# Performance work log

Hardware: AMD Instinct MI355X
Metric: run time of the kernel (lower is better)

Reference implementation:

```python
import jax, jax.numpy as jnp
import numpy as np

SPACE = 63
STRIDE = 2
TEMP = 0.07
W_CHAR, W_WORD, W_PHRASE, W_IDEA = 1.0, 0.5, 0.1, 0.1


def setup_inputs() -> dict:
    key = jax.random.key(0)
    ks = jax.random.split(key, 6)
    B, S, V, D = 8, 4096, 256, 512
    return {
        "logits": jax.random.normal(ks[0], (B, S, V), jnp.float32),
        "word_preds": jax.random.normal(ks[1], (B, D, S // STRIDE), jnp.float32),
        "char_features": jax.random.normal(ks[2], (B, D, S), jnp.float32),
        "contrastive_2": jax.random.normal(ks[3], (B, 128, 1024), jnp.float32),
        "contrastive_3": jax.random.normal(ks[4], (B, 128, 256), jnp.float32),
        "targets": jax.random.randint(ks[5], (B, S), 0, V, jnp.int32),
        "mask": jnp.ones((B, S), jnp.float32),
    }


def _info_nce(emb, temp=TEMP):
    # emb: (B, dim, L). Anchors = even positions, positives = odd positions.
    B, dim, L = emb.shape
    n_pairs = L // 2
    a = emb[:, :, 0:2 * n_pairs:2].transpose(0, 2, 1).reshape(-1, dim)
    p = emb[:, :, 1:2 * n_pairs:2].transpose(0, 2, 1).reshape(-1, dim)
    a = a / jnp.maximum(jnp.linalg.norm(a, axis=1, keepdims=True), 1e-12)
    p = p / jnp.maximum(jnp.linalg.norm(p, axis=1, keepdims=True), 1e-12)
    logits = (a @ p.T) / temp  # (n, n)
    n = logits.shape[0]
    logp = jax.nn.log_softmax(logits, axis=1)
    idx = jnp.arange(n)
    return -jnp.mean(logp[idx, idx])


def _word_span_loss(word_preds, char_features, targets, stride=STRIDE):
    # Segment-mean over spans between consecutive spaces; MSE vs gathered preds.
    B, D, S = char_features.shape
    Wlen = word_preds.shape[2]
    nseg = S + 2  # segment k in [1, n_spaces-1] = span after the k-th space; last slot = junk
    space = targets == SPACE
    cs = jnp.cumsum(space.astype(jnp.int32), axis=1)  # inclusive space count
    seg = jnp.where(space, nseg - 1, cs)          # non-space chars -> span id
    seg_sp = jnp.where(space, cs, nseg - 1)       # space positions -> their space index k
    t_idx = jnp.arange(S, dtype=jnp.int32)

    def per_batch(feats, seg_b, seg_sp_b):
        sums = jax.ops.segment_sum(feats.T, seg_b, num_segments=nseg)  # (nseg, D)
        cnts = jax.ops.segment_sum(jnp.ones((S,), feats.dtype), seg_b, num_segments=nseg)
        pos = jnp.full((nseg,), S, jnp.int32).at[seg_sp_b].set(t_idx)  # position of k-th space
        return sums, cnts, pos

    sums, cnts, pos = jax.vmap(per_batch)(char_features, seg, seg_sp)
    n_sp = cs[:, -1]  # (B,)
    k = jnp.arange(nseg)[None, :]
    valid = (k >= 1) & (k <= n_sp[:, None] - 1) & (cnts > 0) & ((pos // stride) < Wlen)
    means = jax.lax.stop_gradient(sums / jnp.maximum(cnts, 1.0)[..., None])  # target.detach()
    wp = jnp.clip(pos // stride, 0, Wlen - 1)  # (B, nseg)
    preds = jnp.take_along_axis(word_preds.transpose(0, 2, 1), wp[:, :, None], axis=1)  # (B,nseg,D)
    mse = jnp.mean((preds - means) ** 2, axis=-1)  # per-span F.mse_loss (mean over feat dim)
    tot = jnp.sum(jnp.where(valid, mse, 0.0))
    cnt = jnp.sum(valid).astype(mse.dtype)
    return jnp.where(cnt > 0, tot / jnp.maximum(cnt, 1.0), 0.0)


def reference(logits, word_preds, char_features, contrastive_2, contrastive_3, targets, mask):
    # char CE with mask
    logp = jax.nn.log_softmax(logits, axis=-1)
    ce = -jnp.take_along_axis(logp, targets[..., None].astype(jnp.int32), axis=-1)[..., 0]
    n = jnp.sum(mask)
    char_loss = jnp.where(n > 0, jnp.sum(ce * mask) / jnp.maximum(n, 1.0), jnp.mean(ce))
    word_loss = _word_span_loss(word_preds, char_features, targets)
    phrase_loss = _info_nce(contrastive_2)
    idea_loss = _info_nce(contrastive_3)
    return (W_CHAR * char_loss + W_WORD * word_loss
            + W_PHRASE * phrase_loss + W_IDEA * idea_loss)
```

## Files before the change

### kernel.cpp

```cpp
#include <hip/hip_runtime.h>

#define SPACE_TOK 63
#define INV_T 14.285714285714286f
#define SA_SCALE 20.609929155556595f
#define LN2F 0.6931471805599453f

typedef __attribute__((ext_vector_type(8))) short bf16x8;
typedef __attribute__((ext_vector_type(4))) float f32x4;

#define O_CECM   0
#define O_CEM    4096
#define O_CEC    8192
#define O_WPART  12288
#define O_WCNT   14336
#define O_PEXP2  14464
#define O_DIAG2  145536
#define O_PEXP3  161920
#define O_DIAG3  194688
#define O_A2     198784
#define SZ_A2    (4096*128*2)
#define O_P2     (O_A2 + SZ_A2)
#define O_A3     (O_P2 + SZ_A2)
#define SZ_A3    (1024*128*2)
#define O_P3     (O_A3 + SZ_A3)

#define SMEM_A 18048

__device__ inline unsigned short f2bf(float x) {
  union { float f; unsigned int u; } c; c.f = x;
  unsigned int r = c.u + 0x7fffu + ((c.u >> 16) & 1u);
  return (unsigned short)(r >> 16);
}

__device__ void norm_body(char* smem, const float* __restrict__ emb, int L,
                          unsigned short* __restrict__ Abf, unsigned short* __restrict__ Pbf,
                          int b, int l0) {
  float (*tile)[33] = (float(*)[33])smem;
  float (*np8)[32]  = (float(*)[32])(smem + 16896);
  float* scl        = (float*)(smem + 16896 + 1024);
  int tid = threadIdx.x;
  int lx = tid & 31, cq = tid >> 5;
  const float* eb = emb + (size_t)b * 128 * L + l0;
  for (int c = cq; c < 128; c += 8) tile[c][lx] = eb[(size_t)c * L + lx];
  __syncthreads();
  {
    float s = 0.f;
    for (int c = cq; c < 128; c += 8) { float x = tile[c][lx]; s += x * x; }
    np8[cq][lx] = s;
  }
  __syncthreads();
  if (tid < 32) {
    float t = 0.f;
#pragma unroll
    for (int g = 0; g < 8; ++g) t += np8[g][tid];
    float nrm = fmaxf(sqrtf(t), 1e-12f);
    scl[tid] = ((tid & 1) ? 1.0f : SA_SCALE) / nrm;
  }
  __syncthreads();
  int c = tid & 127, lh = tid >> 7;
  int half = L >> 1;
  for (int lp = lh; lp < 32; lp += 2) {
    int l = l0 + lp;
    int row = b * half + (l >> 1);
    unsigned short v = f2bf(tile[c][lp] * scl[lp]);
    ((l & 1) ? Pbf : Abf)[(size_t)row * 128 + c] = v;
  }
}

__device__ void ce_body(char* smem, const float* __restrict__ logits,
                        const int* __restrict__ targets, const float* __restrict__ mask,
                        char* ws, int cb) {
  int tid = threadIdx.x;
  int wave = tid >> 6, lane = tid & 63;
  int rbase = cb * 32 + wave * 8;
  float4 v[8];
  float mk[8];
  int tg[8];
#pragma unroll
  for (int rr = 0; rr < 8; ++rr) v[rr] = ((const float4*)logits)[(size_t)(rbase + rr) * 64 + lane];
#pragma unroll
  for (int rr = 0; rr < 8; ++rr) { tg[rr] = targets[rbase + rr]; mk[rr] = mask[rbase + rr]; }
  float aCM = 0.f, aM = 0.f, aC = 0.f;
#pragma unroll
  for (int rr = 0; rr < 8; ++rr) {
    float e = __expf(v[rr].x) + __expf(v[rr].y) + __expf(v[rr].z) + __expf(v[rr].w);
#pragma unroll
    for (int m = 1; m < 64; m <<= 1) e += __shfl_xor(e, m);
    int t = tg[rr];
    int q = t & 3;
    float sel = (q == 0) ? v[rr].x : (q == 1) ? v[rr].y : (q == 2) ? v[rr].z : v[rr].w;
    float xt = __shfl(sel, t >> 2);
    float ce = __logf(e) - xt;
    aCM += ce * mk[rr]; aM += mk[rr]; aC += ce;
  }
  float (*red)[3] = (float(*)[3])smem;
  if (lane == 0) { red[wave][0] = aCM; red[wave][1] = aM; red[wave][2] = aC; }
  __syncthreads();
  if (tid == 0) {
    ((float*)(ws + O_CECM))[cb] = red[0][0] + red[1][0] + red[2][0] + red[3][0];
    ((float*)(ws + O_CEM ))[cb] = red[0][1] + red[1][1] + red[2][1] + red[3][1];
    ((float*)(ws + O_CEC ))[cb] = red[0][2] + red[1][2] + red[2][2] + red[3][2];
  }
}

__global__ void __launch_bounds__(256) fusedA_kernel(const float* __restrict__ logits,
                                                     const int* __restrict__ targets,
                                                     const float* __restrict__ mask,
                                                     const float* __restrict__ c2,
                                                     const float* __restrict__ c3,
                                                     char* __restrict__ ws) {
  extern __shared__ char smem[];
  int bid = blockIdx.x;
  if (bid < 256) {
    norm_body(smem, c2, 1024, (unsigned short*)(ws + O_A2), (unsigned short*)(ws + O_P2),
              bid & 7, (bid >> 3) * 32);
  } else if (bid < 320) {
    int nb = bid - 256;
    norm_body(smem, c3, 256, (unsigned short*)(ws + O_A3), (unsigned short*)(ws + O_P3),
              nb & 7, (nb >> 3) * 32);
  } else {
    ce_body(smem, logits, targets, mask, ws, bid - 320);
  }
}

__global__ void __launch_bounds__(256) word_kernel(const float* __restrict__ wp,
                                                   const float* __restrict__ cf,
                                                   const int* __restrict__ targets,
                                                   char* __restrict__ ws) {
  __shared__ int sc[256];
  __shared__ int splist[1024];
  __shared__ int snext_sh;
  __shared__ float wacc[4];
  int tid = threadIdx.x;
  int w = blockIdx.x;
  int z = w & 15, tq = (w >> 4) & 3, b = w >> 6;
  const int* tb = targets + b * 4096;
  int tbase = tq * 1024;
  int4 tok = ((const int4*)(tb + tbase))[tid];
  int f0 = (tok.x == SPACE_TOK), f1 = (tok.y == SPACE_TOK),
      f2 = (tok.z == SPACE_TOK), f3 = (tok.w == SPACE_TOK);
  int cnt = f0 + f1 + f2 + f3;
  sc[tid] = cnt;
  __syncthreads();
  for (int off = 1; off < 256; off <<= 1) {
    int v = (tid >= off) ? sc[tid - off] : 0;
    __syncthreads();
    sc[tid] += v;
    __syncthreads();
  }
  int base = sc[tid] - cnt;
  int p = tbase + tid * 4;
  if (f0) splist[base++] = p;
  if (f1) splist[base++] = p + 1;
  if (f2) splist[base++] = p + 2;
  if (f3) splist[base++] = p + 3;
  int m = sc[255];
  if (tid == 0) snext_sh = -1;
  __syncthreads();
  if (m > 0) {
    for (int wstart = tbase + 1024; wstart < 4096 && snext_sh < 0; wstart += 1024) {
      int t = wstart + tid * 4;
      int4 tk = ((const int4*)tb)[t >> 2];
      int found = 0x7fffffff;
      if (tk.x == SPACE_TOK) found = t;
      else if (tk.y == SPACE_TOK) found = t + 1;
      else if (tk.z == SPACE_TOK) found = t + 2;
      else if (tk.w == SPACE_TOK) found = t + 3;
#pragma unroll
      for (int mm = 1; mm < 64; mm <<= 1) found = min(found, __shfl_xor(found, mm));
      if ((tid & 63) == 0) sc[tid >> 6] = found;
      __syncthreads();
      if (tid == 0) {
        int f = min(min(sc[0], sc[1]), min(sc[2], sc[3]));
        if (f != 0x7fffffff) snext_sh = f;
      }
      __syncthreads();
    }
  }
  int snext = snext_sh;
  int wave = tid >> 6, lane = tid & 63;
  int dbase = z * 32 + wave * 8;
  const float* r0 = cf + ((size_t)(b * 512 + dbase)) * 4096;
  float myacc = 0.f;
  float lcnt = 0.f;
  for (int i = 0; i < m; ++i) {
    int t0 = splist[i];
    int t1 = (i + 1 < m) ? splist[i + 1] : snext;
    if (t1 < 0) break;
    int seglen = t1 - t0 - 1;
    if (seglen <= 0) continue;
    lcnt += 1.0f;
    int wpos = t0 >> 1;
    float invc = 1.0f / (float)seglen;
    int c0 = (t0 + 1) >> 2;
    int c1 = (t1 + 3) >> 2;
    float s0 = 0.f, s1 = 0.f, s2 = 0.f, s3 = 0.f, s4 = 0.f, s5 = 0.f, s6 = 0.f, s7 = 0.f;
    for (int c = c0 + lane; c < c1; c += 64) {
      int tbp = c << 2;
      float4 v0 = *(const float4*)(r0 + 0 * 4096 + tbp);
      float4 v1 = *(const float4*)(r0 + 1 * 4096 + tbp);
      float4 v2 = *(const float4*)(r0 + 2 * 4096 + tbp);
      float4 v3 = *(const float4*)(r0 + 3 * 4096 + tbp);
      float4 v4 = *(const float4*)(r0 + 4 * 4096 + tbp);
      float4 v5 = *(const float4*)(r0 + 5 * 4096 + tbp);
      float4 v6 = *(const float4*)(r0 + 6 * 4096 + tbp);
      float4 v7 = *(const float4*)(r0 + 7 * 4096 + tbp);
      float m0 = (tbp + 0 > t0 && tbp + 0 < t1) ? 1.f : 0.f;
      float m1 = (tbp + 1 > t0 && tbp + 1 < t1) ? 1.f : 0.f;
      float m2 = (tbp + 2 > t0 && tbp + 2 < t1) ? 1.f : 0.f;
      float m3 = (tbp + 3 > t0 && tbp + 3 < t1) ? 1.f : 0.f;
      s0 += v0.x * m0 + v0.y * m1 + v0.z * m2 + v0.w * m3;
      s1 += v1.x * m0 + v1.y * m1 + v1.z * m2 + v1.w * m3;
      s2 += v2.x * m0 + v2.y * m1 + v2.z * m2 + v2.w * m3;
      s3 += v3.x * m0 + v3.y * m1 + v3.z * m2 + v3.w * m3;
      s4 += v4.x * m0 + v4.y * m1 + v4.z * m2 + v4.w * m3;
      s5 += v5.x * m0 + v5.y * m1 + v5.z * m2 + v5.w * m3;
      s6 += v6.x * m0 + v6.y * m1 + v6.z * m2 + v6.w * m3;
      s7 += v7.x * m0 + v7.y * m1 + v7.z * m2 + v7.w * m3;
    }
#pragma unroll
    for (int mm = 1; mm < 64; mm <<= 1) {
      s0 += __shfl_xor(s0, mm); s1 += __shfl_xor(s1, mm);
      s2 += __shfl_xor(s2, mm); s3 += __shfl_xor(s3, mm);
      s4 += __shfl_xor(s4, mm); s5 += __shfl_xor(s5, mm);
      s6 += __shfl_xor(s6, mm); s7 += __shfl_xor(s7, mm);
    }
    if (lane < 8) {
      float sv = (lane == 0) ? s0 : (lane == 1) ? s1 : (lane == 2) ? s2 : (lane == 3) ? s3
               : (lane == 4) ? s4 : (lane == 5) ? s5 : (lane == 6) ? s6 : s7;
      float mean = sv * invc;
      float pred = wp[((size_t)(b * 512 + dbase + lane)) * 2048 + wpos];
      float diff = pred - mean;
      myacc += diff * diff;
    }
  }
#pragma unroll
  for (int mm = 1; mm < 8; mm <<= 1) myacc += __shfl_xor(myacc, mm);
  if (lane == 0) wacc[wave] = myacc;
  __syncthreads();
  if (tid == 0) {
    ((float*)(ws + O_WPART))[w] = (wacc[0] + wacc[1] + wacc[2] + wacc[3]) * (1.0f / 512.0f);
    if (z == 0) ((float*)(ws + O_WCNT))[w >> 4] = lcnt;
  }
}

__device__ void nce_body(char* smem, const unsigned short* __restrict__ A,
                         const unsigned short* __restrict__ P, int n, int sliceJ,
                         int blk_i, int s, float* __restrict__ pexp,
                         float* __restrict__ diag) {
  int tid = threadIdx.x;
  int wave = tid >> 6, lane = tid & 63;
  int col = lane & 15, quad = lane >> 4;
  int I0 = blk_i * 16;
  const unsigned short* Ap = A + (size_t)(I0 + col) * 128 + quad * 8;
  bf16x8 a0 = *(const bf16x8*)(Ap);
  bf16x8 a1 = *(const bf16x8*)(Ap + 32);
  bf16x8 a2 = *(const bf16x8*)(Ap + 64);
  bf16x8 a3 = *(const bf16x8*)(Ap + 96);
  float rl0 = 0.f, rl1 = 0.f, rl2 = 0.f, rl3 = 0.f;
  float dcap = 0.f;
  int perW = sliceJ >> 2;
  int J0w = s * sliceJ + wave * perW, Jend = J0w + perW;
#pragma unroll 2
  for (int J = J0w; J < Jend; J += 16) {
    const unsigned short* Pp = P + (size_t)(J + col) * 128 + quad * 8;
    bf16x8 b0 = *(const bf16x8*)(Pp);
    bf16x8 b1 = *(const bf16x8*)(Pp + 32);
    bf16x8 b2 = *(const bf16x8*)(Pp + 64);
    bf16x8 b3 = *(const bf16x8*)(Pp + 96);
    f32x4 cfr = {0.f, 0.f, 0.f, 0.f};
    cfr = __builtin_amdgcn_mfma_f32_16x16x32_bf16(a0, b0, cfr, 0, 0, 0);
    cfr = __builtin_amdgcn_mfma_f32_16x16x32_bf16(a1, b1, cfr, 0, 0, 0);
    cfr = __builtin_amdgcn_mfma_f32_16x16x32_bf16(a2, b2, cfr, 0, 0, 0);
    cfr = __builtin_amdgcn_mfma_f32_16x16x32_bf16(a3, b3, cfr, 0, 0, 0);
    rl0 += exp2f(cfr[0] - SA_SCALE);
    rl1 += exp2f(cfr[1] - SA_SCALE);
    rl2 += exp2f(cfr[2] - SA_SCALE);
    rl3 += exp2f(cfr[3] - SA_SCALE);
    if (J == I0) {
      int r = col - (quad << 2);
      if (r == 0) dcap = cfr[0];
      else if (r == 1) dcap = cfr[1];
      else if (r == 2) dcap = cfr[2];
      else if (r == 3) dcap = cfr[3];
    }
  }
  float (*part)[16][16] = (float(*)[16][16])smem;
  float (*dpart)[16]    = (float(*)[16])(smem + 4096);
  part[wave][(quad << 2) + 0][col] = rl0;
  part[wave][(quad << 2) + 1][col] = rl1;
  part[wave][(quad << 2) + 2][col] = rl2;
  part[wave][(quad << 2) + 3][col] = rl3;
  if (quad == (col >> 2)) dpart[wave][col] = dcap;
  __syncthreads();
  {
    int rrow = tid >> 4, cc = tid & 15;
    float sv = 0.f, d = 0.f;
#pragma unroll
    for (int ww = 0; ww < 4; ++ww) { sv += part[ww][rrow][cc]; d += dpart[ww][rrow]; }
#pragma unroll
    for (int mm = 1; mm < 16; mm <<= 1) sv += __shfl_xor(sv, mm);
    if (cc == 0) {
      pexp[I0 + rrow] = sv;
      if (I0 >= s * sliceJ && I0 < (s + 1) * sliceJ) diag[I0 + rrow] = d;
    }
  }
}

__global__ void __launch_bounds__(256) fusedC_kernel(char* __restrict__ ws) {
  extern __shared__ char smem[];
  int bid = blockIdx.x;
  if (bid < 2048) {
    nce_body(smem, (const unsigned short*)(ws + O_A2), (const unsigned short*)(ws + O_P2),
             4096, 512, bid >> 3, bid & 7,
             (float*)(ws + O_PEXP2) + (bid & 7) * 4096, (float*)(ws + O_DIAG2));
  } else {
    int nb = bid - 2048;
    nce_body(smem, (const unsigned short*)(ws + O_A3), (const unsigned short*)(ws + O_P3),
             1024, 128, nb >> 3, nb & 7,
             (float*)(ws + O_PEXP3) + (nb & 7) * 1024, (float*)(ws + O_DIAG3));
  }
}

__global__ void __launch_bounds__(256) final_kernel(const char* __restrict__ ws,
                                                    float* __restrict__ out) {
  int tid = threadIdx.x;
  int wave = tid >> 6, lane = tid & 63;
  float v[7] = {0.f, 0.f, 0.f, 0.f, 0.f, 0.f, 0.f};
  {
    float4 a = ((const float4*)(ws + O_CECM))[tid];
    float4 bb = ((const float4*)(ws + O_CEM))[tid];
    float4 c = ((const float4*)(ws + O_CEC))[tid];
    v[0] = a.x + a.y + a.z + a.w;
    v[1] = bb.x + bb.y + bb.z + bb.w;
    v[2] = c.x + c.y + c.z + c.w;
  }
  if (tid < 128) {
    float4 wv = ((const float4*)(ws + O_WPART))[tid];
    v[3] = wv.x + wv.y + wv.z + wv.w;
  }
  if (tid < 32) v[4] = ((const float*)(ws + O_WCNT))[tid];
  for (int r4 = tid; r4 < 1024; r4 += 256) {
    float4 S = {0.f, 0.f, 0.f, 0.f};
#pragma unroll
    for (int s = 0; s < 8; ++s) {
      float4 pv = ((const float4*)(ws + O_PEXP2))[s * 1024 + r4];
      S.x += pv.x; S.y += pv.y; S.z += pv.z; S.w += pv.w;
    }
    float4 dg = ((const float4*)(ws + O_DIAG2))[r4];
    v[5] += 4.0f * INV_T + __logf(S.x) + __logf(S.y) + __logf(S.z) + __logf(S.w)
            - LN2F * (dg.x + dg.y + dg.z + dg.w);
  }
  if (tid < 256) {
    int r4 = tid;
    float4 S = {0.f, 0.f, 0.f, 0.f};
#pragma unroll
    for (int s = 0; s < 8; ++s) {
      float4 pv = ((const float4*)(ws + O_PEXP3))[s * 256 + r4];
      S.x += pv.x; S.y += pv.y; S.z += pv.z; S.w += pv.w;
    }
    float4 dg = ((const float4*)(ws + O_DIAG3))[r4];
    v[6] = 4.0f * INV_T + __logf(S.x) + __logf(S.y) + __logf(S.z) + __logf(S.w)
           - LN2F * (dg.x + dg.y + dg.z + dg.w);
  }
#pragma unroll
  for (int j = 0; j < 7; ++j) {
    float x = v[j];
#pragma unroll
    for (int mm = 1; mm < 64; mm <<= 1) x += __shfl_xor(x, mm);
    v[j] = x;
  }
  __shared__ float fr[4][7];
  if (lane == 0)
#pragma unroll
    for (int j = 0; j < 7; ++j) fr[wave][j] = v[j];
  __syncthreads();
  if (tid == 0) {
    float s[7];
#pragma unroll
    for (int j = 0; j < 7; ++j) s[j] = fr[0][j] + fr[1][j] + fr[2][j] + fr[3][j];
    float n = s[1];
    float charL = (n > 0.f) ? (s[0] / fmaxf(n, 1.f)) : (s[2] / 32768.0f);
    float wordL = (s[4] > 0.f) ? (s[3] / fmaxf(s[4], 1.f)) : 0.f;
    out[0] = charL + 0.5f * wordL + 0.1f * (s[5] / 4096.0f) + 0.1f * (s[6] / 1024.0f);
  }
}

extern "C" void kernel_launch(void* const* d_in, const int* in_sizes, int n_in,
                              void* d_out, int out_size, void* d_ws, size_t ws_size,
                              hipStream_t stream) {
  (void)in_sizes; (void)n_in; (void)out_size; (void)ws_size;
  const float* logits        = (const float*)d_in[0];
  const float* word_preds    = (const float*)d_in[1];
  const float* char_features = (const float*)d_in[2];
  const float* c2            = (const float*)d_in[3];
  const float* c3            = (const float*)d_in[4];
  const int*   targets       = (const int*)d_in[5];
  const float* mask          = (const float*)d_in[6];
  float* out = (float*)d_out;
  char* ws = (char*)d_ws;

  fusedA_kernel<<<1344, 256, SMEM_A, stream>>>(logits, targets, mask, c2, c3, ws);
  word_kernel<<<512, 256, 0, stream>>>(word_preds, char_features, targets, ws);
  fusedC_kernel<<<2560, 256, 4480, stream>>>(ws);
  final_kernel<<<1, 256, 0, stream>>>(ws, out);
}
```

Before: 212.5 us.

## Fuse word, NCE and CE work into one kernel and tile bf16 layout for MFMA

Moves the cross-entropy blocks out of the normalisation kernel and merges the word-span loss, both InfoNCE similarity passes and the CE reduction into a single heterogeneous launch. This cuts one kernel launch and lets memory-bound word/CE blocks overlap with MFMA-bound NCE blocks. The normalised bf16 anchor/positive matrices are now written in a 16-row tiled layout, so each lane's MFMA operand loads are contiguous. The LDS partial-sum array is also padded to avoid bank conflicts. The risk is that the fused kernel needs more shared memory per block, which may lower occupancy for the light blocks.

```diff
diff --git a/kernel.cpp b/kernel.cpp
--- a/kernel.cpp
+++ b/kernel.cpp
@@ -17,7 +17,7 @@
 #define O_DIAG2  145536
 #define O_PEXP3  161920
 #define O_DIAG3  194688
-#define O_A2     198784
+#define O_A2     198848
 #define SZ_A2    (4096*128*2)
 #define O_P2     (O_A2 + SZ_A2)
 #define O_A3     (O_P2 + SZ_A2)
@@ -25,6 +25,7 @@
 #define O_P3     (O_A3 + SZ_A3)
 
 #define SMEM_A 18048
+#define SMEM_B 5632
 
 __device__ inline unsigned short f2bf(float x) {
   union { float f; unsigned int u; } c; c.f = x;
@@ -59,54 +60,17 @@
   __syncthreads();
   int c = tid & 127, lh = tid >> 7;
   int half = L >> 1;
+  int k = c >> 5, quad = (c >> 3) & 3, j = c & 7;
   for (int lp = lh; lp < 32; lp += 2) {
     int l = l0 + lp;
     int row = b * half + (l >> 1);
     unsigned short v = f2bf(tile[c][lp] * scl[lp]);
-    ((l & 1) ? Pbf : Abf)[(size_t)row * 128 + c] = v;
-  }
-}
-
-__device__ void ce_body(char* smem, const float* __restrict__ logits,
-                        const int* __restrict__ targets, const float* __restrict__ mask,
-                        char* ws, int cb) {
-  int tid = threadIdx.x;
-  int wave = tid >> 6, lane = tid & 63;
-  int rbase = cb * 32 + wave * 8;
-  float4 v[8];
-  float mk[8];
-  int tg[8];
-#pragma unroll
-  for (int rr = 0; rr < 8; ++rr) v[rr] = ((const float4*)logits)[(size_t)(rbase + rr) * 64 + lane];
-#pragma unroll
-  for (int rr = 0; rr < 8; ++rr) { tg[rr] = targets[rbase + rr]; mk[rr] = mask[rbase + rr]; }
-  float aCM = 0.f, aM = 0.f, aC = 0.f;
-#pragma unroll
-  for (int rr = 0; rr < 8; ++rr) {
-    float e = __expf(v[rr].x) + __expf(v[rr].y) + __expf(v[rr].z) + __expf(v[rr].w);
-#pragma unroll
-    for (int m = 1; m < 64; m <<= 1) e += __shfl_xor(e, m);
-    int t = tg[rr];
-    int q = t & 3;
-    float sel = (q == 0) ? v[rr].x : (q == 1) ? v[rr].y : (q == 2) ? v[rr].z : v[rr].w;
-    float xt = __shfl(sel, t >> 2);
-    float ce = __logf(e) - xt;
-    aCM += ce * mk[rr]; aM += mk[rr]; aC += ce;
-  }
-  float (*red)[3] = (float(*)[3])smem;
-  if (lane == 0) { red[wave][0] = aCM; red[wave][1] = aM; red[wave][2] = aC; }
-  __syncthreads();
-  if (tid == 0) {
-    ((float*)(ws + O_CECM))[cb] = red[0][0] + red[1][0] + red[2][0] + red[3][0];
-    ((float*)(ws + O_CEM ))[cb] = red[0][1] + red[1][1] + red[2][1] + red[3][1];
-    ((float*)(ws + O_CEC ))[cb] = red[0][2] + red[1][2] + red[2][2] + red[3][2];
-  }
-}
-
-__global__ void __launch_bounds__(256) fusedA_kernel(const float* __restrict__ logits,
-                                                     const int* __restrict__ targets,
-                                                     const float* __restrict__ mask,
-                                                     const float* __restrict__ c2,
+    unsigned short* dst = (l & 1) ? Pbf : Abf;
+    dst[(size_t)(row >> 4) * 2048 + k * 512 + ((quad << 4) + (row & 15)) * 8 + j] = v;
+  }
+}
+
+__global__ void __launch_bounds__(256) fusedA_kernel(const float* __restrict__ c2,
                                                      const float* __restrict__ c3,
                                                      char* __restrict__ ws) {
   extern __shared__ char smem[];
@@ -114,25 +78,22 @@
   if (bid < 256) {
     norm_body(smem, c2, 1024, (unsigned short*)(ws + O_A2), (unsigned short*)(ws + O_P2),
               bid & 7, (bid >> 3) * 32);
-  } else if (bid < 320) {
+  } else {
     int nb = bid - 256;
     norm_body(smem, c3, 256, (unsigned short*)(ws + O_A3), (unsigned short*)(ws + O_P3),
               nb & 7, (nb >> 3) * 32);
-  } else {
-    ce_body(smem, logits, targets, mask, ws, bid - 320);
-  }
-}
-
-__global__ void __launch_bounds__(256) word_kernel(const float* __restrict__ wp,
-                                                   const float* __restrict__ cf,
-                                                   const int* __restrict__ targets,
-                                                   char* __restrict__ ws) {
-  __shared__ int sc[256];
-  __shared__ int splist[1024];
-  __shared__ int snext_sh;
-  __shared__ float wacc[4];
+  }
+}
+
+__device__ void word_body(char* smem, const float* __restrict__ wp,
+                          const float* __restrict__ cf,
+                          const int* __restrict__ targets,
+                          char* __restrict__ ws, int w) {
+  int* sc      = (int*)smem;
+  int* splist  = (int*)(smem + 1024);
+  int* snext_sh = (int*)(smem + 5120);
+  float* wacc  = (float*)(smem + 5124);
   int tid = threadIdx.x;
-  int w = blockIdx.x;
   int z = w & 15, tq = (w >> 4) & 3, b = w >> 6;
   const int* tb = targets + b * 4096;
   int tbase = tq * 1024;
@@ -155,10 +116,10 @@
   if (f2) splist[base++] = p + 2;
   if (f3) splist[base++] = p + 3;
   int m = sc[255];
-  if (tid == 0) snext_sh = -1;
+  if (tid == 0) *snext_sh = -1;
   __syncthreads();
   if (m > 0) {
-    for (int wstart = tbase + 1024; wstart < 4096 && snext_sh < 0; wstart += 1024) {
+    for (int wstart = tbase + 1024; wstart < 4096 && *snext_sh < 0; wstart += 1024) {
       int t = wstart + tid * 4;
       int4 tk = ((const int4*)tb)[t >> 2];
       int found = 0x7fffffff;
@@ -172,12 +133,12 @@
       __syncthreads();
       if (tid == 0) {
         int f = min(min(sc[0], sc[1]), min(sc[2], sc[3]));
-        if (f != 0x7fffffff) snext_sh = f;
+        if (f != 0x7fffffff) *snext_sh = f;
       }
       __syncthreads();
     }
   }
-  int snext = snext_sh;
+  int snext = *snext_sh;
   int wave = tid >> 6, lane = tid & 63;
   int dbase = z * 32 + wave * 8;
   const float* r0 = cf + ((size_t)(b * 512 + dbase)) * 4096;
@@ -252,22 +213,22 @@
   int wave = tid >> 6, lane = tid & 63;
   int col = lane & 15, quad = lane >> 4;
   int I0 = blk_i * 16;
-  const unsigned short* Ap = A + (size_t)(I0 + col) * 128 + quad * 8;
-  bf16x8 a0 = *(const bf16x8*)(Ap);
-  bf16x8 a1 = *(const bf16x8*)(Ap + 32);
-  bf16x8 a2 = *(const bf16x8*)(Ap + 64);
-  bf16x8 a3 = *(const bf16x8*)(Ap + 96);
+  const unsigned short* At = A + (size_t)blk_i * 2048 + lane * 8;
+  bf16x8 a0 = *(const bf16x8*)(At);
+  bf16x8 a1 = *(const bf16x8*)(At + 512);
+  bf16x8 a2 = *(const bf16x8*)(At + 1024);
+  bf16x8 a3 = *(const bf16x8*)(At + 1536);
   float rl0 = 0.f, rl1 = 0.f, rl2 = 0.f, rl3 = 0.f;
   float dcap = 0.f;
   int perW = sliceJ >> 2;
   int J0w = s * sliceJ + wave * perW, Jend = J0w + perW;
 #pragma unroll 2
   for (int J = J0w; J < Jend; J += 16) {
-    const unsigned short* Pp = P + (size_t)(J + col) * 128 + quad * 8;
-    bf16x8 b0 = *(const bf16x8*)(Pp);
-    bf16x8 b1 = *(const bf16x8*)(Pp + 32);
-    bf16x8 b2 = *(const bf16x8*)(Pp + 64);
-    bf16x8 b3 = *(const bf16x8*)(Pp + 96);
+    const unsigned short* Pt = P + (size_t)(J >> 4) * 2048 + lane * 8;
+    bf16x8 b0 = *(const bf16x8*)(Pt);
+    bf16x8 b1 = *(const bf16x8*)(Pt + 512);
+    bf16x8 b2 = *(const bf16x8*)(Pt + 1024);
+    bf16x8 b3 = *(const bf16x8*)(Pt + 1536);
     f32x4 cfr = {0.f, 0.f, 0.f, 0.f};
     cfr = __builtin_amdgcn_mfma_f32_16x16x32_bf16(a0, b0, cfr, 0, 0, 0);
     cfr = __builtin_amdgcn_mfma_f32_16x16x32_bf16(a1, b1, cfr, 0, 0, 0);
@@ -285,8 +246,8 @@
       else if (r == 3) dcap = cfr[3];
     }
   }
-  float (*part)[16][16] = (float(*)[16][16])smem;
-  float (*dpart)[16]    = (float(*)[16])(smem + 4096);
+  float (*part)[16][17] = (float(*)[16][17])smem;
+  float (*dpart)[16]    = (float(*)[16])(smem + 4352);
   part[wave][(quad << 2) + 0][col] = rl0;
   part[wave][(quad << 2) + 1][col] = rl1;
   part[wave][(quad << 2) + 2][col] = rl2;
@@ -307,18 +268,64 @@
   }
 }
 
-__global__ void __launch_bounds__(256) fusedC_kernel(char* __restrict__ ws) {
+__device__ void ce_body(char* smem, const float* __restrict__ logits,
+                        const int* __restrict__ targets, const float* __restrict__ mask,
+                        char* ws, int cb) {
+  int tid = threadIdx.x;
+  int wave = tid >> 6, lane = tid & 63;
+  int rbase = cb * 32 + wave * 8;
+  float4 v[8];
+  float mk[8];
+  int tg[8];
+#pragma unroll
+  for (int rr = 0; rr < 8; ++rr) v[rr] = ((const float4*)logits)[(size_t)(rbase + rr) * 64 + lane];
+#pragma unroll
+  for (int rr = 0; rr < 8; ++rr) { tg[rr] = targets[rbase + rr]; mk[rr] = mask[rbase + rr]; }
+  float aCM = 0.f, aM = 0.f, aC = 0.f;
+#pragma unroll
+  for (int rr = 0; rr < 8; ++rr) {
+    float e = __expf(v[rr].x) + __expf(v[rr].y) + __expf(v[rr].z) + __expf(v[rr].w);
+#pragma unroll
+    for (int m = 1; m < 64; m <<= 1) e += __shfl_xor(e, m);
+    int t = tg[rr];
+    int q = t & 3;
+    float sel = (q == 0) ? v[rr].x : (q == 1) ? v[rr].y : (q == 2) ? v[rr].z : v[rr].w;
+    float xt = __shfl(sel, t >> 2);
+    float ce = __logf(e) - xt;
+    aCM += ce * mk[rr]; aM += mk[rr]; aC += ce;
+  }
+  float (*red)[3] = (float(*)[3])smem;
+  if (lane == 0) { red[wave][0] = aCM; red[wave][1] = aM; red[wave][2] = aC; }
+  __syncthreads();
+  if (tid == 0) {
+    ((float*)(ws + O_CECM))[cb] = red[0][0] + red[1][0] + red[2][0] + red[3][0];
+    ((float*)(ws + O_CEM ))[cb] = red[0][1] + red[1][1] + red[2][1] + red[3][1];
+    ((float*)(ws + O_CEC ))[cb] = red[0][2] + red[1][2] + red[2][2] + red[3][2];
+  }
+}
+
+__global__ void __launch_bounds__(256) fusedB_kernel(const float* __restrict__ logits,
+                                                     const float* __restrict__ wp,
+                                                     const float* __restrict__ cf,
+                                                     const int* __restrict__ targets,
+                                                     const float* __restrict__ mask,
+                                                     char* __restrict__ ws) {
   extern __shared__ char smem[];
   int bid = blockIdx.x;
-  if (bid < 2048) {
+  if (bid < 512) {
+    word_body(smem, wp, cf, targets, ws, bid);
+  } else if (bid < 2560) {
+    int nb = bid - 512;
     nce_body(smem, (const unsigned short*)(ws + O_A2), (const unsigned short*)(ws + O_P2),
-             4096, 512, bid >> 3, bid & 7,
-             (float*)(ws + O_PEXP2) + (bid & 7) * 4096, (float*)(ws + O_DIAG2));
-  } else {
-    int nb = bid - 2048;
+             4096, 512, nb >> 3, nb & 7,
+             (float*)(ws + O_PEXP2) + (nb & 7) * 4096, (float*)(ws + O_DIAG2));
+  } else if (bid < 3072) {
+    int nb = bid - 2560;
     nce_body(smem, (const unsigned short*)(ws + O_A3), (const unsigned short*)(ws + O_P3),
              1024, 128, nb >> 3, nb & 7,
              (float*)(ws + O_PEXP3) + (nb & 7) * 1024, (float*)(ws + O_DIAG3));
+  } else {
+    ce_body(smem, logits, targets, mask, ws, bid - 3072);
   }
 }
 
@@ -351,7 +358,7 @@
     v[5] += 4.0f * INV_T + __logf(S.x) + __logf(S.y) + __logf(S.z) + __logf(S.w)
             - LN2F * (dg.x + dg.y + dg.z + dg.w);
   }
-  if (tid < 256) {
+  {
     int r4 = tid;
     float4 S = {0.f, 0.f, 0.f, 0.f};
 #pragma unroll
@@ -400,8 +407,8 @@
   float* out = (float*)d_out;
   char* ws = (char*)d_ws;
 
-  fusedA_kernel<<<1344, 256, SMEM_A, stream>>>(logits, targets, mask, c2, c3, ws);
-  word_kernel<<<512, 256, 0, stream>>>(word_preds, char_features, targets, ws);
-  fusedC_kernel<<<2560, 256, 4480, stream>>>(ws);
+  fusedA_kernel<<<320, 256, SMEM_A, stream>>>(c2, c3, ws);
+  fusedB_kernel<<<4096, 256, SMEM_B, stream>>>(logits, word_preds, char_features,
+                                               targets, mask, ws);
   final_kernel<<<1, 256, 0, stream>>>(ws, out);
 }
```

After: 174.3 us. -18.0%, faster.
